# Optimization experiments

Measured on AMD Instinct MI355X. Metric: run time of the kernel, lower is better.

The kernel has to match this reference:

```python
import jax, jax.numpy as jnp
import numpy as np

H = 32          # num attention heads
D = 128         # head dim
HID = 4096      # hidden size
MIN_R = 1.0     # compress_ratio_min
MAX_R = 3.0     # compress_ratio_max
BASE = 10000.0  # rope_theta


def rotate_half(x):
    x1, x2 = jnp.split(x, 2, axis=-1)
    return jnp.concatenate([-x2, x1], axis=-1)


def ms_poe_cos_sin(seq_len):
    # Per-head compressed positions: t_h = arange(S) / ratio_h
    inv_freq = 1.0 / (BASE ** (jnp.arange(0, D, 2, dtype=jnp.float32) / D))   # [D/2]
    ratio = MIN_R + (MAX_R - MIN_R) * (jnp.arange(H, dtype=jnp.float32) / H)  # [H]
    t = jnp.arange(seq_len, dtype=jnp.float32)[None, :] / ratio[:, None]      # [H,S]
    freqs = t[:, :, None] * inv_freq[None, None, :]                           # [H,S,D/2]
    emb = jnp.concatenate([freqs, freqs], axis=-1)                            # [H,S,D]
    return jnp.cos(emb), jnp.sin(emb)


def setup_inputs() -> dict:
    key = jax.random.key(0)
    ks = jax.random.split(key, 5)
    B, S = 1, 2048
    scale = 0.02
    return {
        "hidden_states": jax.random.normal(ks[0], (B, S, HID), dtype=jnp.float32),
        "position_ids": jnp.broadcast_to(jnp.arange(S, dtype=jnp.int64 if jax.config.jax_enable_x64 else jnp.int32), (B, S)),
        "wq": jax.random.normal(ks[1], (HID, HID), dtype=jnp.float32) * scale,
        "wk": jax.random.normal(ks[2], (HID, HID), dtype=jnp.float32) * scale,
        "wv": jax.random.normal(ks[3], (HID, HID), dtype=jnp.float32) * scale,
        "wo": jax.random.normal(ks[4], (HID, HID), dtype=jnp.float32) * scale,
    }


def reference(hidden_states, position_ids, wq, wk, wv, wo):
    B, S, _ = hidden_states.shape
    dtype = hidden_states.dtype

    # QKV projections (torch Linear: y = x @ W.T), split into heads -> [B,H,S,D]
    q = (hidden_states @ wq.T).reshape(B, S, H, D).transpose(0, 2, 1, 3)
    k = (hidden_states @ wk.T).reshape(B, S, H, D).transpose(0, 2, 1, 3)
    v = (hidden_states @ wv.T).reshape(B, S, H, D).transpose(0, 2, 1, 3)

    # Per-head scaled rotary embedding; head_type='normal' -> reversed head order
    cos, sin = ms_poe_cos_sin(S)                 # [H,S,D]
    order = H - jnp.arange(H) - 1
    cos, sin = cos[order], sin[order]

    # cos[:, position_ids] -> [H,B,S,D] -> transpose(0,1) -> [B,H,S,D]
    cos_p = jnp.transpose(cos[:, position_ids], (1, 0, 2, 3)).astype(dtype)
    sin_p = jnp.transpose(sin[:, position_ids], (1, 0, 2, 3)).astype(dtype)

    q = q * cos_p + rotate_half(q) * sin_p
    # num_key_value_groups == 1 -> sample_rotary_emb is identity; same cos/sin for k
    k = k * cos_p + rotate_half(k) * sin_p

    # Causal softmax attention (eager, as in original)
    scores = jnp.einsum("bhqd,bhkd->bhqk", q, k) / jnp.sqrt(jnp.asarray(D, dtype))
    neg = jnp.finfo(dtype).min
    causal = jnp.where(jnp.tril(jnp.ones((S, S), dtype=bool)), 0.0, neg).astype(dtype)
    scores = scores + causal[None, None]
    attn = jax.nn.softmax(scores, axis=-1)
    out = jnp.einsum("bhqk,bhkd->bhqd", attn, v)  # [B,H,S,D]

    out = out.transpose(0, 2, 1, 3).reshape(B, S, HID)
    return out @ wo.T
```

## Files before the change

### kernel.cpp

```cpp
#include <hip/hip_runtime.h>
#include <math.h>

#define HIDDEN 4096
#define NHEADS 32
#define HEADDIM 128

typedef __attribute__((ext_vector_type(8))) short bf16x8;
typedef __attribute__((ext_vector_type(4))) float f32x4;

#define GLL(g, l) __builtin_amdgcn_global_load_lds( \
    (const __attribute__((address_space(1))) void*)(g), \
    (__attribute__((address_space(3))) void*)(l), 16, 0, 0)

__device__ __forceinline__ unsigned short f2bf(float f) {
  unsigned int u = __float_as_uint(f);
  unsigned int r = (u + 0x7FFFu + ((u >> 16) & 1u)) >> 16;
  return (unsigned short)r;
}
__device__ __forceinline__ float bf2f(unsigned short h) {
  return __uint_as_float(((unsigned int)h) << 16);
}

__global__ __launch_bounds__(256)
void split_bf16(const float* __restrict__ X, unsigned short* __restrict__ H,
                unsigned short* __restrict__ L) {
  const int i = blockIdx.x * 256 + threadIdx.x;
  float4 v = ((const float4*)X)[i];
  ushort4 h, lo;
  const float* vf = (const float*)&v;
  unsigned short* hp = (unsigned short*)&h;
  unsigned short* lp = (unsigned short*)&lo;
#pragma unroll
  for (int j = 0; j < 4; ++j) {
    float f = vf[j];
    unsigned short hb = f2bf(f);
    hp[j] = hb;
    lp[j] = f2bf(f - bf2f(hb));
  }
  ((ushort4*)H)[i] = h;
  ((ushort4*)L)[i] = lo;
}

__global__ __launch_bounds__(256)
void gemm_bf16x3(const unsigned short* __restrict__ Ahi, const unsigned short* __restrict__ Alo,
                 const unsigned short* __restrict__ Bhi, const unsigned short* __restrict__ Blo,
                 float* __restrict__ C, int M, int N, int K) {
  __shared__ unsigned short lds[4 * 4096];
  const int tid = threadIdx.x;
  const int bm = blockIdx.y * 128;
  const int bn = blockIdx.x * 128;
  const int w = tid >> 6, l = tid & 63;
  const int wr = (w >> 1) * 64, wc = (w & 1) * 64;
  const int lr = l & 15, lc = l >> 4;

  f32x4 acc[4][4];
#pragma unroll
  for (int m = 0; m < 4; ++m)
#pragma unroll
    for (int n = 0; n < 4; ++n) acc[m][n] = (f32x4){0.f, 0.f, 0.f, 0.f};

  const int p0 = tid, p1 = tid + 256;
  const int r0 = p0 >> 2, c0 = (p0 & 3) ^ (r0 & 3);
  const int r1 = p1 >> 2, c1 = (p1 & 3) ^ (r1 & 3);
  const size_t a0 = (size_t)(bm + r0) * K + c0 * 8;
  const size_t a1 = (size_t)(bm + r1) * K + c1 * 8;
  const size_t b0 = (size_t)(bn + r0) * K + c0 * 8;
  const size_t b1 = (size_t)(bn + r1) * K + c1 * 8;
  unsigned short* lp0 = &lds[p0 * 8];
  unsigned short* lp1 = &lds[p1 * 8];

  const int fa = (lc ^ (lr & 3)) * 8;
  int aoff[4], boff[4];
#pragma unroll
  for (int m = 0; m < 4; ++m) aoff[m] = (wr + m * 16 + lr) * 32 + fa;
#pragma unroll
  for (int n = 0; n < 4; ++n) boff[n] = (wc + n * 16 + lr) * 32 + fa;

  for (int kt = 0; kt < K; kt += 32) {
    GLL(Ahi + a0 + kt, lp0);
    GLL(Ahi + a1 + kt, lp1);
    GLL(Alo + a0 + kt, lp0 + 4096);
    GLL(Alo + a1 + kt, lp1 + 4096);
    GLL(Bhi + b0 + kt, lp0 + 8192);
    GLL(Bhi + b1 + kt, lp1 + 8192);
    GLL(Blo + b0 + kt, lp0 + 12288);
    GLL(Blo + b1 + kt, lp1 + 12288);
    __syncthreads();

    bf16x8 ah[4], al[4], bh[4], bl[4];
#pragma unroll
    for (int m = 0; m < 4; ++m) {
      ah[m] = *(const bf16x8*)&lds[aoff[m]];
      al[m] = *(const bf16x8*)&lds[4096 + aoff[m]];
    }
#pragma unroll
    for (int n = 0; n < 4; ++n) {
      bh[n] = *(const bf16x8*)&lds[8192 + boff[n]];
      bl[n] = *(const bf16x8*)&lds[12288 + boff[n]];
    }
#pragma unroll
    for (int m = 0; m < 4; ++m)
#pragma unroll
      for (int n = 0; n < 4; ++n) {
        acc[m][n] = __builtin_amdgcn_mfma_f32_16x16x32_bf16(ah[m], bh[n], acc[m][n], 0, 0, 0);
        acc[m][n] = __builtin_amdgcn_mfma_f32_16x16x32_bf16(ah[m], bl[n], acc[m][n], 0, 0, 0);
        acc[m][n] = __builtin_amdgcn_mfma_f32_16x16x32_bf16(al[m], bh[n], acc[m][n], 0, 0, 0);
      }
    __syncthreads();
  }

#pragma unroll
  for (int m = 0; m < 4; ++m) {
    const int row0 = bm + wr + m * 16 + lc * 4;
#pragma unroll
    for (int n = 0; n < 4; ++n) {
      const int col = bn + wc + n * 16 + lr;
      float* cp = C + (size_t)row0 * N + col;
#pragma unroll
      for (int j = 0; j < 4; ++j) cp[(size_t)j * N] = acc[m][n][j];
    }
  }
}

__global__ __launch_bounds__(256)
void gemm_nt(const float* __restrict__ A, const float* __restrict__ B,
             float* __restrict__ C, int M, int N, int K) {
  __shared__ float As[16][128];
  __shared__ float Bs[16][128];
  const int tid = threadIdx.x;
  const int bm = blockIdx.y * 128;
  const int bn = blockIdx.x * 128;
  const int ty = tid >> 4;
  const int tx = tid & 15;
  const int lrow = tid >> 1;
  const int lkq = (tid & 1) * 4;

  float acc[8][8];
#pragma unroll
  for (int i = 0; i < 8; ++i)
#pragma unroll
    for (int j = 0; j < 8; ++j) acc[i][j] = 0.f;

  const float* Ap = A + (size_t)(bm + lrow) * K + lkq;
  const float* Bp = B + (size_t)(bn + lrow) * K + lkq;

  for (int kt = 0; kt < K; kt += 16) {
    float4 a0 = *(const float4*)(Ap + kt);
    float4 a1 = *(const float4*)(Ap + kt + 8);
    float4 b0 = *(const float4*)(Bp + kt);
    float4 b1 = *(const float4*)(Bp + kt + 8);
    __syncthreads();
    As[lkq + 0][lrow] = a0.x; As[lkq + 1][lrow] = a0.y;
    As[lkq + 2][lrow] = a0.z; As[lkq + 3][lrow] = a0.w;
    As[lkq + 8][lrow] = a1.x; As[lkq + 9][lrow] = a1.y;
    As[lkq +10][lrow] = a1.z; As[lkq +11][lrow] = a1.w;
    Bs[lkq + 0][lrow] = b0.x; Bs[lkq + 1][lrow] = b0.y;
    Bs[lkq + 2][lrow] = b0.z; Bs[lkq + 3][lrow] = b0.w;
    Bs[lkq + 8][lrow] = b1.x; Bs[lkq + 9][lrow] = b1.y;
    Bs[lkq +10][lrow] = b1.z; Bs[lkq +11][lrow] = b1.w;
    __syncthreads();
#pragma unroll
    for (int k = 0; k < 16; ++k) {
      float a[8], b[8];
      *(float4*)&a[0] = *(const float4*)&As[k][ty * 8];
      *(float4*)&a[4] = *(const float4*)&As[k][ty * 8 + 4];
      *(float4*)&b[0] = *(const float4*)&Bs[k][tx * 8];
      *(float4*)&b[4] = *(const float4*)&Bs[k][tx * 8 + 4];
#pragma unroll
      for (int i = 0; i < 8; ++i)
#pragma unroll
        for (int j = 0; j < 8; ++j) acc[i][j] = fmaf(a[i], b[j], acc[i][j]);
    }
  }
  float* Cp = C + (size_t)(bm + ty * 8) * N + bn + tx * 8;
#pragma unroll
  for (int i = 0; i < 8; ++i) {
    *(float4*)(Cp + (size_t)i * N) = *(float4*)&acc[i][0];
    *(float4*)(Cp + (size_t)i * N + 4) = *(float4*)&acc[i][4];
  }
}

__global__ __launch_bounds__(256)
void rope_kernel(float* __restrict__ Q, float* __restrict__ Kc,
                 const int* __restrict__ pos_ids, int S) {
  const int row = blockIdx.x * 4 + (threadIdx.x >> 6);
  const int j = threadIdx.x & 63;
  const int s = row >> 5;
  const int h = row & 31;
  const int pos = pos_ids[s];
  const int hr = NHEADS - 1 - h;
  const float ratio = 1.0f + 2.0f * ((float)hr / 32.0f);
  const float t = (float)pos / ratio;
  const float inv = (float)exp(-0.143911568312127875 * (double)j);
  const float ang = t * inv;
  float sn, cs;
  sincosf(ang, &sn, &cs);
  const size_t base = (size_t)s * HIDDEN + (size_t)h * HEADDIM + j;
  const float q0 = Q[base], q1 = Q[base + 64];
  Q[base] = q0 * cs - q1 * sn;
  Q[base + 64] = q1 * cs + q0 * sn;
  const float k0 = Kc[base], k1 = Kc[base + 64];
  Kc[base] = k0 * cs - k1 * sn;
  Kc[base + 64] = k1 * cs + k0 * sn;
}

__global__ __launch_bounds__(256)
void attn_kernel(const float* __restrict__ Q, const float* __restrict__ K,
                 const float* __restrict__ V, float* __restrict__ O, int S) {
  __shared__ float Ks[32 * 128];
  __shared__ float Vs[32 * 128];
  const int h = blockIdx.y;
  const int nqb = S >> 5;
  const int tid = threadIdx.x;
  const int wave = tid >> 6, lane = tid & 63;
  const int r = lane >> 3, c = lane & 7;
  const int strow = tid >> 3, stc = tid & 7;
  const float scale = 0.08838834764831845f;

  for (int half = 0; half < 2; ++half) {
    const int qb = half ? (nqb - 1 - (int)blockIdx.x) : (int)blockIdx.x;
    const int qrow = qb * 32 + wave * 8 + r;
    const float* qp = Q + (size_t)qrow * HIDDEN + h * HEADDIM;
    float qf[16];
#pragma unroll
    for (int i = 0; i < 4; ++i)
      *(float4*)&qf[i * 4] = *(const float4*)(qp + c * 4 + 32 * i);
    float o[16];
#pragma unroll
    for (int i = 0; i < 16; ++i) o[i] = 0.f;
    float m = -INFINITY, l = 0.f;
    const int ntiles = qb + 1;

    const float* kg = K + (size_t)strow * HIDDEN + h * HEADDIM;
    const float* vg = V + (size_t)strow * HIDDEN + h * HEADDIM;
    float4 kreg[4], vreg[4];
#pragma unroll
    for (int jj = 0; jj < 4; ++jj) {
      kreg[jj] = *(const float4*)(kg + (stc + jj * 8) * 4);
      vreg[jj] = *(const float4*)(vg + (stc + jj * 8) * 4);
    }
    for (int t = 0; t < ntiles; ++t) {
      __syncthreads();
#pragma unroll
      for (int jj = 0; jj < 4; ++jj) {
        *(float4*)&Ks[strow * 128 + (stc + jj * 8) * 4] = kreg[jj];
        *(float4*)&Vs[strow * 128 + (stc + jj * 8) * 4] = vreg[jj];
      }
      if (t + 1 < ntiles) {
        const float* kg2 = kg + (size_t)(t + 1) * 32 * HIDDEN;
        const float* vg2 = vg + (size_t)(t + 1) * 32 * HIDDEN;
#pragma unroll
        for (int jj = 0; jj < 4; ++jj) {
          kreg[jj] = *(const float4*)(kg2 + (stc + jj * 8) * 4);
          vreg[jj] = *(const float4*)(vg2 + (stc + jj * 8) * 4);
        }
      }
      __syncthreads();

      const int kb = t * 32;
      float sv[32];
#pragma unroll
      for (int kk = 0; kk < 32; ++kk) {
        const float* kr = &Ks[kk * 128 + c * 4];
        float kv[16];
#pragma unroll
        for (int i = 0; i < 4; ++i)
          *(float4*)&kv[i * 4] = *(const float4*)(kr + 32 * i);
        float d0 = 0.f, d1 = 0.f, d2 = 0.f, d3 = 0.f;
#pragma unroll
        for (int i = 0; i < 4; ++i) {
          d0 = fmaf(qf[i], kv[i], d0);
          d1 = fmaf(qf[4 + i], kv[4 + i], d1);
          d2 = fmaf(qf[8 + i], kv[8 + i], d2);
          d3 = fmaf(qf[12 + i], kv[12 + i], d3);
        }
        float d = (d0 + d1) + (d2 + d3);
        d += __shfl_xor(d, 1);
        d += __shfl_xor(d, 2);
        d += __shfl_xor(d, 4);
        sv[kk] = (kb + kk <= qrow) ? d * scale : -INFINITY;
      }
      float tmax = -INFINITY;
#pragma unroll
      for (int kk = 0; kk < 32; ++kk) tmax = fmaxf(tmax, sv[kk]);
      const float mnew = fmaxf(m, tmax);
      const float corr = __expf(m - mnew);
#pragma unroll
      for (int i = 0; i < 16; ++i) o[i] *= corr;
      float psum = 0.f;
#pragma unroll
      for (int kk = 0; kk < 32; ++kk) {
        const float p = __expf(sv[kk] - mnew);
        psum += p;
        const float* vr = &Vs[kk * 128 + c * 4];
        float vv[16];
#pragma unroll
        for (int i = 0; i < 4; ++i)
          *(float4*)&vv[i * 4] = *(const float4*)(vr + 32 * i);
#pragma unroll
        for (int i = 0; i < 16; ++i) o[i] = fmaf(p, vv[i], o[i]);
      }
      l = l * corr + psum;
      m = mnew;
    }
    const float invl = 1.0f / l;
    float* op = O + (size_t)qrow * HIDDEN + h * HEADDIM + c * 4;
#pragma unroll
    for (int i = 0; i < 4; ++i) {
      float4 ov;
      ov.x = o[i * 4 + 0] * invl;
      ov.y = o[i * 4 + 1] * invl;
      ov.z = o[i * 4 + 2] * invl;
      ov.w = o[i * 4 + 3] * invl;
      *(float4*)(op + 32 * i) = ov;
    }
  }
}

extern "C" void kernel_launch(void* const* d_in, const int* in_sizes, int n_in,
                              void* d_out, int out_size, void* d_ws, size_t ws_size,
                              hipStream_t stream) {
  const float* hs = (const float*)d_in[0];
  const int* pos = (const int*)d_in[1];
  const float* wq = (const float*)d_in[2];
  const float* wk = (const float*)d_in[3];
  const float* wv = (const float*)d_in[4];
  const float* wo = (const float*)d_in[5];
  float* out = (float*)d_out;

  const int S = in_sizes[0] / HIDDEN;
  const size_t planeF = (size_t)S * HIDDEN * sizeof(float);
  const size_t planeH = (size_t)S * HIDDEN * sizeof(short);
  const size_t wplaneH = (size_t)HIDDEN * HIDDEN * sizeof(short);
  const size_t needed = 3 * planeF + 4 * planeH + 8 * wplaneH;

  char* wp = (char*)d_ws;
  float* q = (float*)wp;   wp += planeF;
  float* k = (float*)wp;   wp += planeF;
  float* ao = (float*)wp;  wp += planeF;
  float* v = out;

  dim3 mg(HIDDEN / 128, S / 128);
  const int nh = S * HIDDEN;
  const int nw = HIDDEN * HIDDEN;

  if (ws_size >= needed) {
    unsigned short* hs_hi = (unsigned short*)wp;  wp += planeH;
    unsigned short* hs_lo = (unsigned short*)wp;  wp += planeH;
    unsigned short* ao_hi = (unsigned short*)wp;  wp += planeH;
    unsigned short* ao_lo = (unsigned short*)wp;  wp += planeH;
    unsigned short* wqh = (unsigned short*)wp;  wp += wplaneH;
    unsigned short* wql = (unsigned short*)wp;  wp += wplaneH;
    unsigned short* wkh = (unsigned short*)wp;  wp += wplaneH;
    unsigned short* wkl = (unsigned short*)wp;  wp += wplaneH;
    unsigned short* wvh = (unsigned short*)wp;  wp += wplaneH;
    unsigned short* wvl = (unsigned short*)wp;  wp += wplaneH;
    unsigned short* woh = (unsigned short*)wp;  wp += wplaneH;
    unsigned short* wol = (unsigned short*)wp;  wp += wplaneH;

    split_bf16<<<nh / 1024, 256, 0, stream>>>(hs, hs_hi, hs_lo);
    split_bf16<<<nw / 1024, 256, 0, stream>>>(wq, wqh, wql);
    split_bf16<<<nw / 1024, 256, 0, stream>>>(wk, wkh, wkl);
    split_bf16<<<nw / 1024, 256, 0, stream>>>(wv, wvh, wvl);
    split_bf16<<<nw / 1024, 256, 0, stream>>>(wo, woh, wol);

    gemm_bf16x3<<<mg, 256, 0, stream>>>(hs_hi, hs_lo, wqh, wql, q, S, HIDDEN, HIDDEN);
    gemm_bf16x3<<<mg, 256, 0, stream>>>(hs_hi, hs_lo, wkh, wkl, k, S, HIDDEN, HIDDEN);
    gemm_bf16x3<<<mg, 256, 0, stream>>>(hs_hi, hs_lo, wvh, wvl, v, S, HIDDEN, HIDDEN);

    rope_kernel<<<(S * NHEADS) / 4, 256, 0, stream>>>(q, k, pos, S);
    attn_kernel<<<dim3(S / 64, NHEADS), 256, 0, stream>>>(q, k, v, ao, S);

    split_bf16<<<nh / 1024, 256, 0, stream>>>(ao, ao_hi, ao_lo);
    gemm_bf16x3<<<mg, 256, 0, stream>>>(ao_hi, ao_lo, woh, wol, out, S, HIDDEN, HIDDEN);
  } else {
    gemm_nt<<<mg, 256, 0, stream>>>(hs, wq, q, S, HIDDEN, HIDDEN);
    gemm_nt<<<mg, 256, 0, stream>>>(hs, wk, k, S, HIDDEN, HIDDEN);
    gemm_nt<<<mg, 256, 0, stream>>>(hs, wv, v, S, HIDDEN, HIDDEN);
    rope_kernel<<<(S * NHEADS) / 4, 256, 0, stream>>>(q, k, pos, S);
    attn_kernel<<<dim3(S / 64, NHEADS), 256, 0, stream>>>(q, k, v, ao, S);
    gemm_nt<<<mg, 256, 0, stream>>>(ao, wo, out, S, HIDDEN, HIDDEN);
  }
}
```

Baseline: 4.729 ms.

## Double-buffer LDS in GEMM and attention with async global-to-LDS prefetch

The bf16x3 GEMM gets a second LDS buffer so the next K-tile is fetched with global_load_lds while MFMAs run on the current one. This removes one barrier per iteration and changes the XOR swizzle to cut LDS bank conflicts. The attention kernel stops staging K/V through registers and uses double-buffered direct global-to-LDS loads instead. Doubling LDS use may lower occupancy, and the lack of explicit vmcnt waits before the barrier relies on compiler-inserted waits for correctness.

Result: faster. 4.458 ms (-5.7%).

```diff
diff --git a/kernel.cpp b/kernel.cpp
--- a/kernel.cpp
+++ b/kernel.cpp
@@ -45,7 +45,7 @@
 void gemm_bf16x3(const unsigned short* __restrict__ Ahi, const unsigned short* __restrict__ Alo,
                  const unsigned short* __restrict__ Bhi, const unsigned short* __restrict__ Blo,
                  float* __restrict__ C, int M, int N, int K) {
-  __shared__ unsigned short lds[4 * 4096];
+  __shared__ unsigned short lds[2][4][4096];
   const int tid = threadIdx.x;
   const int bm = blockIdx.y * 128;
   const int bn = blockIdx.x * 128;
@@ -60,43 +60,49 @@
     for (int n = 0; n < 4; ++n) acc[m][n] = (f32x4){0.f, 0.f, 0.f, 0.f};
 
   const int p0 = tid, p1 = tid + 256;
-  const int r0 = p0 >> 2, c0 = (p0 & 3) ^ (r0 & 3);
-  const int r1 = p1 >> 2, c1 = (p1 & 3) ^ (r1 & 3);
+  const int r0 = p0 >> 2, c0 = (p0 & 3) ^ ((p0 >> 3) & 3);
+  const int r1 = p1 >> 2, c1 = (p1 & 3) ^ ((p1 >> 3) & 3);
   const size_t a0 = (size_t)(bm + r0) * K + c0 * 8;
   const size_t a1 = (size_t)(bm + r1) * K + c1 * 8;
   const size_t b0 = (size_t)(bn + r0) * K + c0 * 8;
   const size_t b1 = (size_t)(bn + r1) * K + c1 * 8;
-  unsigned short* lp0 = &lds[p0 * 8];
-  unsigned short* lp1 = &lds[p1 * 8];
-
-  const int fa = (lc ^ (lr & 3)) * 8;
+
+  const int pos = (lc ^ ((lr >> 1) & 3)) * 8;
   int aoff[4], boff[4];
 #pragma unroll
-  for (int m = 0; m < 4; ++m) aoff[m] = (wr + m * 16 + lr) * 32 + fa;
-#pragma unroll
-  for (int n = 0; n < 4; ++n) boff[n] = (wc + n * 16 + lr) * 32 + fa;
-
+  for (int m = 0; m < 4; ++m) aoff[m] = (wr + m * 16 + lr) * 32 + pos;
+#pragma unroll
+  for (int n = 0; n < 4; ++n) boff[n] = (wc + n * 16 + lr) * 32 + pos;
+
+#define STAGE(b, kt)                                  \
+  do {                                                \
+    unsigned short* Lb = &lds[(b)][0][0];             \
+    GLL(Ahi + a0 + (kt), Lb + p0 * 8);                \
+    GLL(Ahi + a1 + (kt), Lb + p1 * 8);                \
+    GLL(Alo + a0 + (kt), Lb + 4096 + p0 * 8);         \
+    GLL(Alo + a1 + (kt), Lb + 4096 + p1 * 8);         \
+    GLL(Bhi + b0 + (kt), Lb + 8192 + p0 * 8);         \
+    GLL(Bhi + b1 + (kt), Lb + 8192 + p1 * 8);         \
+    GLL(Blo + b0 + (kt), Lb + 12288 + p0 * 8);        \
+    GLL(Blo + b1 + (kt), Lb + 12288 + p1 * 8);        \
+  } while (0)
+
+  STAGE(0, 0);
   for (int kt = 0; kt < K; kt += 32) {
-    GLL(Ahi + a0 + kt, lp0);
-    GLL(Ahi + a1 + kt, lp1);
-    GLL(Alo + a0 + kt, lp0 + 4096);
-    GLL(Alo + a1 + kt, lp1 + 4096);
-    GLL(Bhi + b0 + kt, lp0 + 8192);
-    GLL(Bhi + b1 + kt, lp1 + 8192);
-    GLL(Blo + b0 + kt, lp0 + 12288);
-    GLL(Blo + b1 + kt, lp1 + 12288);
+    const int b = (kt >> 5) & 1;
     __syncthreads();
-
+    if (kt + 32 < K) STAGE(b ^ 1, kt + 32);
+    const unsigned short* Lb = &lds[b][0][0];
     bf16x8 ah[4], al[4], bh[4], bl[4];
 #pragma unroll
     for (int m = 0; m < 4; ++m) {
-      ah[m] = *(const bf16x8*)&lds[aoff[m]];
-      al[m] = *(const bf16x8*)&lds[4096 + aoff[m]];
+      ah[m] = *(const bf16x8*)(Lb + aoff[m]);
+      al[m] = *(const bf16x8*)(Lb + 4096 + aoff[m]);
     }
 #pragma unroll
     for (int n = 0; n < 4; ++n) {
-      bh[n] = *(const bf16x8*)&lds[8192 + boff[n]];
-      bl[n] = *(const bf16x8*)&lds[12288 + boff[n]];
+      bh[n] = *(const bf16x8*)(Lb + 8192 + boff[n]);
+      bl[n] = *(const bf16x8*)(Lb + 12288 + boff[n]);
     }
 #pragma unroll
     for (int m = 0; m < 4; ++m)
@@ -106,8 +112,8 @@
         acc[m][n] = __builtin_amdgcn_mfma_f32_16x16x32_bf16(ah[m], bl[n], acc[m][n], 0, 0, 0);
         acc[m][n] = __builtin_amdgcn_mfma_f32_16x16x32_bf16(al[m], bh[n], acc[m][n], 0, 0, 0);
       }
-    __syncthreads();
-  }
+  }
+#undef STAGE
 
 #pragma unroll
   for (int m = 0; m < 4; ++m) {
@@ -207,15 +213,27 @@
 __global__ __launch_bounds__(256)
 void attn_kernel(const float* __restrict__ Q, const float* __restrict__ K,
                  const float* __restrict__ V, float* __restrict__ O, int S) {
-  __shared__ float Ks[32 * 128];
-  __shared__ float Vs[32 * 128];
+  __shared__ float Ks[2][32 * 128];
+  __shared__ float Vs[2][32 * 128];
   const int h = blockIdx.y;
   const int nqb = S >> 5;
   const int tid = threadIdx.x;
   const int wave = tid >> 6, lane = tid & 63;
   const int r = lane >> 3, c = lane & 7;
-  const int strow = tid >> 3, stc = tid & 7;
   const float scale = 0.08838834764831845f;
+  const float* Kh = K + (size_t)h * HEADDIM;
+  const float* Vh = V + (size_t)h * HEADDIM;
+
+#define ASTAGE(b, kb)                                                        \
+  do {                                                                       \
+    _Pragma("unroll")                                                        \
+    for (int i = 0; i < 4; ++i) {                                            \
+      const int p = i * 256 + tid;                                           \
+      const int row = p >> 5, c4 = p & 31;                                   \
+      GLL(Kh + (size_t)((kb) + row) * HIDDEN + c4 * 4, &Ks[(b)][p * 4]);     \
+      GLL(Vh + (size_t)((kb) + row) * HIDDEN + c4 * 4, &Vs[(b)][p * 4]);     \
+    }                                                                        \
+  } while (0)
 
   for (int half = 0; half < 2; ++half) {
     const int qb = half ? (nqb - 1 - (int)blockIdx.x) : (int)blockIdx.x;
@@ -228,40 +246,22 @@
     float o[16];
 #pragma unroll
     for (int i = 0; i < 16; ++i) o[i] = 0.f;
-    float m = -INFINITY, l = 0.f;
-    const int ntiles = qb + 1;
-
-    const float* kg = K + (size_t)strow * HIDDEN + h * HEADDIM;
-    const float* vg = V + (size_t)strow * HIDDEN + h * HEADDIM;
-    float4 kreg[4], vreg[4];
-#pragma unroll
-    for (int jj = 0; jj < 4; ++jj) {
-      kreg[jj] = *(const float4*)(kg + (stc + jj * 8) * 4);
-      vreg[jj] = *(const float4*)(vg + (stc + jj * 8) * 4);
-    }
-    for (int t = 0; t < ntiles; ++t) {
+    float m = -INFINITY, lsum = 0.f;
+    const int nt = qb + 1;
+
+    __syncthreads();
+    ASTAGE(0, 0);
+    for (int t = 0; t < nt; ++t) {
       __syncthreads();
-#pragma unroll
-      for (int jj = 0; jj < 4; ++jj) {
-        *(float4*)&Ks[strow * 128 + (stc + jj * 8) * 4] = kreg[jj];
-        *(float4*)&Vs[strow * 128 + (stc + jj * 8) * 4] = vreg[jj];
-      }
-      if (t + 1 < ntiles) {
-        const float* kg2 = kg + (size_t)(t + 1) * 32 * HIDDEN;
-        const float* vg2 = vg + (size_t)(t + 1) * 32 * HIDDEN;
-#pragma unroll
-        for (int jj = 0; jj < 4; ++jj) {
-          kreg[jj] = *(const float4*)(kg2 + (stc + jj * 8) * 4);
-          vreg[jj] = *(const float4*)(vg2 + (stc + jj * 8) * 4);
-        }
-      }
-      __syncthreads();
-
+      if (t + 1 < nt) ASTAGE((t + 1) & 1, (t + 1) * 32);
+      const float* Kb = Ks[t & 1];
+      const float* Vb = Vs[t & 1];
       const int kb = t * 32;
+
       float sv[32];
 #pragma unroll
       for (int kk = 0; kk < 32; ++kk) {
-        const float* kr = &Ks[kk * 128 + c * 4];
+        const float* kr = Kb + kk * 128 + c * 4;
         float kv[16];
 #pragma unroll
         for (int i = 0; i < 4; ++i)
@@ -292,7 +292,7 @@
       for (int kk = 0; kk < 32; ++kk) {
         const float p = __expf(sv[kk] - mnew);
         psum += p;
-        const float* vr = &Vs[kk * 128 + c * 4];
+        const float* vr = Vb + kk * 128 + c * 4;
         float vv[16];
 #pragma unroll
         for (int i = 0; i < 4; ++i)
@@ -300,10 +300,10 @@
 #pragma unroll
         for (int i = 0; i < 16; ++i) o[i] = fmaf(p, vv[i], o[i]);
       }
-      l = l * corr + psum;
+      lsum = lsum * corr + psum;
       m = mnew;
     }
-    const float invl = 1.0f / l;
+    const float invl = 1.0f / lsum;
     float* op = O + (size_t)qrow * HIDDEN + h * HEADDIM + c * 4;
 #pragma unroll
     for (int i = 0; i < 4; ++i) {
@@ -315,6 +315,7 @@
       *(float4*)(op + 32 * i) = ov;
     }
   }
+#undef ASTAGE
 }
 
 extern "C" void kernel_launch(void* const* d_in, const int* in_sizes, int n_in,
```
